# Performance work log

Hardware: AMD Instinct MI355X
Metric: run time of the kernel (lower is better)

## Reference

```python
import jax, jax.numpy as jnp
import numpy as np

B_, L_, D_MODEL = 2, 4096, 1024
D_STATE, D_CONV, D_INNER = 64, 4, 2048
EPS = 1.1920929e-07  # torch.finfo(float32).eps, nn.RMSNorm default


def setup_inputs() -> dict:
    key = jax.random.key(0)
    ks = jax.random.split(key, 8)
    s = 0.02
    x = jax.random.normal(ks[0], (B_, L_, D_MODEL), jnp.float32)
    W_in = jax.random.normal(ks[1], (D_MODEL, 2 * D_INNER), jnp.float32) * s
    conv_w = jax.random.normal(ks[2], (D_INNER, 1, D_CONV), jnp.float32) * s  # depthwise (O,I/g,K)
    conv_b = jnp.zeros((D_INNER,), jnp.float32)
    W_x = jax.random.normal(ks[3], (D_INNER, 2 * D_STATE + D_INNER), jnp.float32) * s
    W_dt = jax.random.normal(ks[4], (D_INNER, D_INNER), jnp.float32) * s
    b_dt = jnp.zeros((D_INNER,), jnp.float32)
    A_log = jnp.log(jnp.tile(jnp.arange(1, D_STATE + 1, dtype=jnp.float32)[None, :], (D_INNER, 1)))
    D_param = jnp.ones((D_INNER,), jnp.float32)
    W_out = jax.random.normal(ks[5], (D_INNER, D_MODEL), jnp.float32) * s
    norm_w = jnp.ones((D_INNER,), jnp.float32)
    return dict(x=x, W_in=W_in, conv_w=conv_w, conv_b=conv_b, W_x=W_x, W_dt=W_dt,
                b_dt=b_dt, A_log=A_log, D_param=D_param, W_out=W_out, norm_w=norm_w)


def selective_scan(x_conv, dt, A, B_ssm, C_ssm, D_param):
    # x_conv,dt: (B,L,d_inner); A:(d_inner,d_state); B_ssm,C_ssm:(B,L,d_state)
    dt = jax.nn.softplus(dt)

    def step(h, inp):
        dt_t, B_t, C_t, x_t = inp  # (B,di),(B,ds),(B,ds),(B,di)
        dA = jnp.exp(dt_t[:, :, None] * A[None, :, :])           # (B,di,ds)
        h = dA * h + (dt_t * x_t)[:, :, None] * B_t[:, None, :]  # (B,di,ds)
        y = jnp.einsum('bds,bs->bd', h, C_t)                     # (B,di)
        return h, y

    h0 = jnp.zeros((x_conv.shape[0], A.shape[0], A.shape[1]), x_conv.dtype)
    xs = (jnp.moveaxis(dt, 1, 0), jnp.moveaxis(B_ssm, 1, 0),
          jnp.moveaxis(C_ssm, 1, 0), jnp.moveaxis(x_conv, 1, 0))
    _, ys = jax.lax.scan(step, h0, xs)
    y = jnp.moveaxis(ys, 0, 1)  # (B,L,d_inner)
    return y + x_conv * D_param[None, None, :]


def reference(x, W_in, conv_w, conv_b, W_x, W_dt, b_dt, A_log, D_param, W_out, norm_w):
    xz = x @ W_in                                    # (B,L,2*d_inner)
    x_ssm, z = jnp.split(xz, 2, axis=-1)
    # causal depthwise conv1d: left-pad d_conv-1 == torch pad-both-then-slice[:L]
    xc = jnp.swapaxes(x_ssm, 1, 2)                   # (B,d_inner,L)
    xc = jax.lax.conv_general_dilated(
        xc, conv_w, window_strides=(1,), padding=[(D_CONV - 1, 0)],
        dimension_numbers=('NCH', 'OIH', 'NCH'), feature_group_count=D_INNER)
    xc = xc + conv_b[None, :, None]
    xc = jax.nn.silu(jnp.swapaxes(xc, 1, 2))         # (B,L,d_inner)
    dbc = xc @ W_x                                   # (B,L,2*d_state+d_inner)
    B_ssm = dbc[..., :D_STATE]
    C_ssm = dbc[..., D_STATE:2 * D_STATE]
    dt = dbc[..., 2 * D_STATE:] @ W_dt + b_dt
    A = -jnp.exp(A_log)
    y = selective_scan(xc, dt, A, B_ssm, C_ssm, D_param)
    # RMSNorm then gate
    y = y * jax.lax.rsqrt(jnp.mean(y * y, axis=-1, keepdims=True) + EPS) * norm_w
    y = y * jax.nn.silu(z)
    return y @ W_out
```

## Files before the change

### kernel.cpp

```cpp
#include <hip/hip_runtime.h>
#include <hip/hip_bf16.h>

#define L_SEQ   4096
#define DMODEL  1024
#define DINNER  2048
#define DSTATE  64
#define NB      2
#define DPB     128
#define NROWS   (NB * L_SEQ)

typedef unsigned short u16;
typedef __attribute__((ext_vector_type(8))) short bf16x8;
typedef __attribute__((ext_vector_type(4))) float f32x4;

__device__ __forceinline__ float silu_f(float x)  { return x / (1.f + __expf(-x)); }
__device__ __forceinline__ float softplus_f(float x) {
    return x > 15.f ? x : __logf(1.f + __expf(x));
}
__device__ __forceinline__ float bf2f(u16 u) { return __uint_as_float(((unsigned)u) << 16); }
__device__ __forceinline__ u16 f2bf(float f) {
    __hip_bfloat16 h = __float2bfloat16(f);
    return *reinterpret_cast<u16*>(&h);
}
__device__ __forceinline__ unsigned pack2(float a, float b) {
    return (unsigned)f2bf(a) | ((unsigned)f2bf(b) << 16);
}

__global__ __launch_bounds__(256) void f32_to_bf16_kernel(
    const float* __restrict__ in, u16* __restrict__ out)
{
    const int i = (blockIdx.x * 256 + threadIdx.x) * 4;
    float4 v = *reinterpret_cast<const float4*>(in + i);
    ushort4 o;
    o.x = f2bf(v.x); o.y = f2bf(v.y); o.z = f2bf(v.z); o.w = f2bf(v.w);
    *reinterpret_cast<ushort4*>(out + i) = o;
}

__global__ __launch_bounds__(256) void transpose_bf16_kernel(
    const float* __restrict__ W, u16* __restrict__ Wt, int K, int N)
{
    __shared__ float t[32][33];
    const int n0 = blockIdx.x * 32, k0 = blockIdx.y * 32;
    const int tx = threadIdx.x & 31, ty = threadIdx.x >> 5;
    #pragma unroll
    for (int i = 0; i < 32; i += 8)
        t[ty + i][tx] = W[(size_t)(k0 + ty + i) * N + n0 + tx];
    __syncthreads();
    #pragma unroll
    for (int i = 0; i < 32; i += 8)
        Wt[(size_t)(n0 + ty + i) * K + k0 + tx] = f2bf(t[tx][ty + i]);
}

__global__ __launch_bounds__(256) void bias_cat_kernel(
    const float* __restrict__ b_dt, float* __restrict__ bias)
{
    const int i = blockIdx.x * 256 + threadIdx.x;
    if (i < 128 + DINNER) bias[i] = (i < 128) ? 0.f : b_dt[i - 128];
}

template <typename TC>
__global__ __launch_bounds__(256) void mfma_gemm(
    const u16* __restrict__ A, int lda,
    const u16* __restrict__ Bt, int ldb,
    TC* __restrict__ C, int ldc,
    int K, const float* __restrict__ bias)
{
    __shared__ u16 As[128 * 32];
    __shared__ u16 Bs[128 * 32];
    const int tid  = threadIdx.x;
    const int lane = tid & 63;
    const int w    = tid >> 6;
    const int wm   = w >> 1, wn = w & 1;

    const int gx = gridDim.x;
    const int nwg = gx * gridDim.y;
    int wg = blockIdx.y * gx + blockIdx.x;
    if ((nwg & 7) == 0) wg = (wg & 7) * (nwg >> 3) + (wg >> 3);
    const int bm = (wg / gx) * 128, bn = (wg % gx) * 128;

    const int lr = lane & 15, lk = lane >> 4;
    const int srow  = lane >> 2;
    const int scolb = (lane & 3) * 16;
    const size_t ldaB = (size_t)lda * 2, ldbB = (size_t)ldb * 2;

    const char* Ab = (const char*)A + (size_t)bm * ldaB;
    const char* Bb = (const char*)Bt + (size_t)bn * ldbB;
    char* AsB = (char*)As;
    char* BsB = (char*)Bs;

    f32x4 acc[4][4] = {};

    for (int k0 = 0; k0 < K; k0 += 32) {
        const size_t kb = (size_t)k0 * 2;
        #pragma unroll
        for (int i = 0; i < 2; ++i) {
            const int row = i * 64 + w * 16 + srow;
            __builtin_amdgcn_global_load_lds(
                (const __attribute__((address_space(1))) void*)(Ab + (size_t)row * ldaB + kb + scolb),
                (__attribute__((address_space(3))) void*)(AsB + i * 4096 + w * 1024),
                16, 0, 0);
            __builtin_amdgcn_global_load_lds(
                (const __attribute__((address_space(1))) void*)(Bb + (size_t)row * ldbB + kb + scolb),
                (__attribute__((address_space(3))) void*)(BsB + i * 4096 + w * 1024),
                16, 0, 0);
        }
        __syncthreads();
        bf16x8 a[4], b[4];
        #pragma unroll
        for (int mi = 0; mi < 4; ++mi)
            a[mi] = *reinterpret_cast<const bf16x8*>(&As[(wm * 64 + mi * 16 + lr) * 32 + lk * 8]);
        #pragma unroll
        for (int ni = 0; ni < 4; ++ni)
            b[ni] = *reinterpret_cast<const bf16x8*>(&Bs[(wn * 64 + ni * 16 + lr) * 32 + lk * 8]);
        #pragma unroll
        for (int mi = 0; mi < 4; ++mi)
            #pragma unroll
            for (int ni = 0; ni < 4; ++ni)
                acc[mi][ni] = __builtin_amdgcn_mfma_f32_16x16x32_bf16(a[mi], b[ni], acc[mi][ni], 0, 0, 0);
        __syncthreads();
    }

    float bv[4];
    if (bias) {
        #pragma unroll
        for (int ni = 0; ni < 4; ++ni) bv[ni] = bias[bn + wn * 64 + ni * 16 + lr];
    }
    #pragma unroll
    for (int mi = 0; mi < 4; ++mi) {
        #pragma unroll
        for (int ni = 0; ni < 4; ++ni) {
            #pragma unroll
            for (int r = 0; r < 4; ++r) {
                const int row = bm + wm * 64 + mi * 16 + lk * 4 + r;
                const int col = bn + wn * 64 + ni * 16 + lr;
                float v = acc[mi][ni][r];
                if (bias) v += bv[ni];
                if constexpr (sizeof(TC) == 4) C[(size_t)row * ldc + col] = v;
                else                           C[(size_t)row * ldc + col] = f2bf(v);
            }
        }
    }
}

__global__ __launch_bounds__(256) void conv_silu_kernel(
    const u16* __restrict__ xz, const float* __restrict__ cw,
    const float* __restrict__ cb, u16* __restrict__ xc)
{
    const int idx8 = blockIdx.x * 256 + threadIdx.x;
    const int db  = (idx8 & 255) << 3;
    const int row = idx8 >> 8;
    const int l   = row & (L_SEQ - 1);

    float v[4][8];
    #pragma unroll
    for (int k = 0; k < 4; ++k) {
        const int ll = l - 3 + k;
        if (ll >= 0) {
            uint4 u = *reinterpret_cast<const uint4*>(xz + (size_t)(row - 3 + k) * 4096 + db);
            v[k][0]=bf2f((u16)(u.x&0xffff)); v[k][1]=bf2f((u16)(u.x>>16));
            v[k][2]=bf2f((u16)(u.y&0xffff)); v[k][3]=bf2f((u16)(u.y>>16));
            v[k][4]=bf2f((u16)(u.z&0xffff)); v[k][5]=bf2f((u16)(u.z>>16));
            v[k][6]=bf2f((u16)(u.w&0xffff)); v[k][7]=bf2f((u16)(u.w>>16));
        } else {
            #pragma unroll
            for (int j = 0; j < 8; ++j) v[k][j] = 0.f;
        }
    }
    float acc[8];
    {
        float4 c0 = *reinterpret_cast<const float4*>(cb + db);
        float4 c1 = *reinterpret_cast<const float4*>(cb + db + 4);
        acc[0]=c0.x; acc[1]=c0.y; acc[2]=c0.z; acc[3]=c0.w;
        acc[4]=c1.x; acc[5]=c1.y; acc[6]=c1.z; acc[7]=c1.w;
    }
    #pragma unroll
    for (int j = 0; j < 8; ++j) {
        const float4 wv = reinterpret_cast<const float4*>(cw)[db + j];
        acc[j] = fmaf(v[0][j], wv.x, acc[j]);
        acc[j] = fmaf(v[1][j], wv.y, acc[j]);
        acc[j] = fmaf(v[2][j], wv.z, acc[j]);
        acc[j] = fmaf(v[3][j], wv.w, acc[j]);
    }
    uint4 o;
    o.x = pack2(silu_f(acc[0]), silu_f(acc[1]));
    o.y = pack2(silu_f(acc[2]), silu_f(acc[3]));
    o.z = pack2(silu_f(acc[4]), silu_f(acc[5]));
    o.w = pack2(silu_f(acc[6]), silu_f(acc[7]));
    *reinterpret_cast<uint4*>(xc + (size_t)row * 2048 + db) = o;
}


__device__ __forceinline__ int a_pattern_check_half(
    const float* A_log, int d, int base, float& A0)
{
    A0 = -__expf(A_log[d * DSTATE]);
    int ok = 1;
    #pragma unroll
    for (int j = 0; j < 32; ++j) {
        const int s = base + j;
        const float As = -__expf(A_log[d * DSTATE + s]);
        ok &= (fabsf(As - A0 * (float)(s + 1)) <= 1e-3f * (float)(s + 1));
    }
    return ok;
}

#define UNPACK8(dstp, u)  do {                                             \
    float4 _a, _b;                                                         \
    _a.x=bf2f((u16)((u).x&0xffff)); _a.y=bf2f((u16)((u).x>>16));           \
    _a.z=bf2f((u16)((u).y&0xffff)); _a.w=bf2f((u16)((u).y>>16));           \
    _b.x=bf2f((u16)((u).z&0xffff)); _b.y=bf2f((u16)((u).z>>16));           \
    _b.z=bf2f((u16)((u).w&0xffff)); _b.w=bf2f((u16)((u).w>>16));           \
    *reinterpret_cast<float4*>(dstp) = _a;                                 \
    *reinterpret_cast<float4*>((dstp) + 4) = _b;                           \
} while (0)

#define UNPACK8_SP(dstp, u)  do {                                          \
    float4 _a, _b;                                                         \
    _a.x=softplus_f(bf2f((u16)((u).x&0xffff)));                            \
    _a.y=softplus_f(bf2f((u16)((u).x>>16)));                               \
    _a.z=softplus_f(bf2f((u16)((u).y&0xffff)));                            \
    _a.w=softplus_f(bf2f((u16)((u).y>>16)));                               \
    _b.x=softplus_f(bf2f((u16)((u).z&0xffff)));                            \
    _b.y=softplus_f(bf2f((u16)((u).z>>16)));                               \
    _b.z=softplus_f(bf2f((u16)((u).w&0xffff)));                            \
    _b.w=softplus_f(bf2f((u16)((u).w>>16)));                               \
    *reinterpret_cast<float4*>(dstp) = _a;                                 \
    *reinterpret_cast<float4*>((dstp) + 4) = _b;                           \
} while (0)

__global__ __launch_bounds__(256) void scan_phase1(
    const u16* __restrict__ xc,
    const u16* __restrict__ dbc,
    const float* __restrict__ A_log,
    float* __restrict__ hend, float* __restrict__ sumdt,
    int nchunk, int chunk)
{
    const int tid  = threadIdx.x;
    const int dl   = tid >> 1, half = tid & 1;
    const int base = half * 32;
    const int d0   = blockIdx.x * DPB;
    const int d    = d0 + dl;
    const int c = blockIdx.y, b = blockIdx.z;
    const int t0 = c * chunk;
    const size_t bL = (size_t)b * L_SEQ;

    __shared__ float dts_s[16][132];
    __shared__ float xcs_s[16][132];
    __shared__ float Bs_s[16][68];

    float A0;
    int fast = a_pattern_check_half(A_log, d, base, A0);
    fast = __syncthreads_and(fast);

    float h[32];
    #pragma unroll
    for (int j = 0; j < 32; ++j) h[j] = 0.f;
    float sd = 0.f;

    for (int ts = 0; ts < chunk; ts += 16) {
        __syncthreads();
        {
            const int rr = tid >> 4, cc = (tid & 15) * 8;
            const size_t row = bL + t0 + ts + rr;
            uint4 v = *reinterpret_cast<const uint4*>(dbc + row * 2176 + 128 + d0 + cc);
            UNPACK8_SP(&dts_s[rr][cc], v);
            uint4 u = *reinterpret_cast<const uint4*>(xc + row * 2048 + d0 + cc);
            UNPACK8(&xcs_s[rr][cc], u);
        }
        if (tid < 128) {
            const int rr = tid >> 3, cc = (tid & 7) * 8;
            const size_t row = bL + t0 + ts + rr;
            uint4 v = *reinterpret_cast<const uint4*>(dbc + row * 2176 + cc);
            UNPACK8(&Bs_s[rr][cc], v);
        }
        __syncthreads();
        if (fast) {
            for (int r = 0; r < 16; ++r) {
                const float dts = dts_s[r][dl];
                const float xv  = xcs_s[r][dl];
                const float dtx = dts * xv;
                sd += dts;
                const float q  = __expf(A0 * dts);
                const float q2 = q * q, q4 = q2 * q2;
                const float q8 = q4 * q4, q16 = q8 * q8, q32 = q16 * q16;
                const float qb = half ? q32 : 1.f;
                float p0 = qb * q, p1 = qb * q2, p2 = p1 * q, p3 = qb * q4;
                #pragma unroll
                for (int g = 0; g < 8; ++g) {
                    const float4 Bv = *reinterpret_cast<const float4*>(&Bs_s[r][base + g * 4]);
                    h[g*4+0] = fmaf(p0, h[g*4+0], dtx * Bv.x);
                    h[g*4+1] = fmaf(p1, h[g*4+1], dtx * Bv.y);
                    h[g*4+2] = fmaf(p2, h[g*4+2], dtx * Bv.z);
                    h[g*4+3] = fmaf(p3, h[g*4+3], dtx * Bv.w);
                    p0 *= q4; p1 *= q4; p2 *= q4; p3 *= q4;
                }
            }
        } else {
            for (int r = 0; r < 16; ++r) {
                const float dts = dts_s[r][dl];
                const float xv  = xcs_s[r][dl];
                const float dtx = dts * xv;
                sd += dts;
                #pragma unroll
                for (int j = 0; j < 32; ++j) {
                    const float a = __expf(-__expf(A_log[d * DSTATE + base + j]) * dts);
                    h[j] = fmaf(a, h[j], dtx * Bs_s[r][base + j]);
                }
            }
        }
    }
    const size_t cb64 = ((size_t)b * nchunk + c) * DSTATE;
    #pragma unroll
    for (int j = 0; j < 32; ++j) hend[(cb64 + base + j) * DINNER + d] = h[j];
    if (half == 0) sumdt[((size_t)b * nchunk + c) * DINNER + d] = sd;
}

__global__ __launch_bounds__(256) void scan_phase2(
    float* __restrict__ hbuf, const float* __restrict__ sumdt,
    const float* __restrict__ A_log, int nchunk)
{
    const int idx = blockIdx.x * 256 + threadIdx.x;
    const int d = idx & (DINNER - 1);
    const int s = (idx >> 11) & (DSTATE - 1);
    const int b = idx >> 17;

    const float A = -__expf(A_log[d * DSTATE + s]);
    float h = 0.f;
    for (int c = 0; c < nchunk; ++c) {
        const size_t off = (((size_t)b * nchunk + c) * DSTATE + s) * DINNER + d;
        const float he = hbuf[off];
        const float ap = __expf(A * sumdt[((size_t)b * nchunk + c) * DINNER + d]);
        hbuf[off] = h;
        h = fmaf(ap, h, he);
    }
}

__global__ __launch_bounds__(256) void scan_phase3(
    u16* __restrict__ xc,
    const u16* __restrict__ dbc,
    const float* __restrict__ A_log,
    const float* __restrict__ hinit,
    const float* __restrict__ D_param,
    int nchunk, int chunk)
{
    const int tid  = threadIdx.x;
    const int dl   = tid >> 1, half = tid & 1;
    const int base = half * 32;
    const int d0   = blockIdx.x * DPB;
    const int d    = d0 + dl;
    const int c = blockIdx.y, b = blockIdx.z;
    const int t0 = c * chunk;
    const size_t bL = (size_t)b * L_SEQ;

    __shared__ float dts_s[16][132];
    __shared__ float xcs_s[16][132];
    __shared__ float BCs[16][132];

    float A0;
    int fast = a_pattern_check_half(A_log, d, base, A0);
    fast = __syncthreads_and(fast);

    float h[32];
    {
        const size_t cb64 = ((size_t)b * nchunk + c) * DSTATE;
        #pragma unroll
        for (int j = 0; j < 32; ++j) h[j] = hinit[(cb64 + base + j) * DINNER + d];
    }
    const float Dp = D_param[d];

    for (int ts = 0; ts < chunk; ts += 16) {
        __syncthreads();
        {
            const int rr = tid >> 4, cc = (tid & 15) * 8;
            const size_t row = bL + t0 + ts + rr;
            uint4 v = *reinterpret_cast<const uint4*>(dbc + row * 2176 + 128 + d0 + cc);
            UNPACK8_SP(&dts_s[rr][cc], v);
            uint4 u = *reinterpret_cast<const uint4*>(xc + row * 2048 + d0 + cc);
            UNPACK8(&xcs_s[rr][cc], u);
            uint4 w = *reinterpret_cast<const uint4*>(dbc + row * 2176 + cc);
            UNPACK8(&BCs[rr][cc], w);
        }
        __syncthreads();
        if (fast) {
            for (int r = 0; r < 16; ++r) {
                const float dts = dts_s[r][dl];
                const float xv  = xcs_s[r][dl];
                const float dtx = dts * xv;
                const float q  = __expf(A0 * dts);
                const float q2 = q * q, q4 = q2 * q2;
                const float q8 = q4 * q4, q16 = q8 * q8, q32 = q16 * q16;
                const float qb = half ? q32 : 1.f;
                float p0 = qb * q, p1 = qb * q2, p2 = p1 * q, p3 = qb * q4;
                float y = 0.f;
                #pragma unroll
                for (int g = 0; g < 8; ++g) {
                    const float4 Bv = *reinterpret_cast<const float4*>(&BCs[r][base + g * 4]);
                    const float4 Cv = *reinterpret_cast<const float4*>(&BCs[r][64 + base + g * 4]);
                    h[g*4+0] = fmaf(p0, h[g*4+0], dtx * Bv.x);  y = fmaf(h[g*4+0], Cv.x, y);
                    h[g*4+1] = fmaf(p1, h[g*4+1], dtx * Bv.y);  y = fmaf(h[g*4+1], Cv.y, y);
                    h[g*4+2] = fmaf(p2, h[g*4+2], dtx * Bv.z);  y = fmaf(h[g*4+2], Cv.z, y);
                    h[g*4+3] = fmaf(p3, h[g*4+3], dtx * Bv.w);  y = fmaf(h[g*4+3], Cv.w, y);
                    p0 *= q4; p1 *= q4; p2 *= q4; p3 *= q4;
                }
                const float yt = y + __shfl_xor(y, 1, 64);
                if (half == 0) {
                    const size_t row = bL + t0 + ts + r;
                    xc[row * 2048 + d] = f2bf(fmaf(xv, Dp, yt));
                }
            }
        } else {
            for (int r = 0; r < 16; ++r) {
                const float dts = dts_s[r][dl];
                const float xv  = xcs_s[r][dl];
                const float dtx = dts * xv;
                float y = 0.f;
                #pragma unroll
                for (int j = 0; j < 32; ++j) {
                    const float a = __expf(-__expf(A_log[d * DSTATE + base + j]) * dts);
                    h[j] = fmaf(a, h[j], dtx * BCs[r][base + j]);
                    y = fmaf(h[j], BCs[r][64 + base + j], y);
                }
                const float yt = y + __shfl_xor(y, 1, 64);
                if (half == 0) {
                    const size_t row = bL + t0 + ts + r;
                    xc[row * 2048 + d] = f2bf(fmaf(xv, Dp, yt));
                }
            }
        }
    }
}

__global__ __launch_bounds__(256) void rms_gate_kernel(
    u16* __restrict__ y, const u16* __restrict__ xz,
    const float* __restrict__ norm_w)
{
    const int row = blockIdx.x;
    const int tid = threadIdx.x;
    const size_t ybase = (size_t)row * DINNER;
    const size_t zbase = (size_t)row * 4096 + DINNER;
    const int i8 = tid * 8;

    float yv[8];
    {
        uint4 u = *reinterpret_cast<const uint4*>(y + ybase + i8);
        yv[0]=bf2f((u16)(u.x&0xffff)); yv[1]=bf2f((u16)(u.x>>16));
        yv[2]=bf2f((u16)(u.y&0xffff)); yv[3]=bf2f((u16)(u.y>>16));
        yv[4]=bf2f((u16)(u.z&0xffff)); yv[5]=bf2f((u16)(u.z>>16));
        yv[6]=bf2f((u16)(u.w&0xffff)); yv[7]=bf2f((u16)(u.w>>16));
    }
    float ss = 0.f;
    #pragma unroll
    for (int j = 0; j < 8; ++j) ss = fmaf(yv[j], yv[j], ss);
    #pragma unroll
    for (int off = 32; off > 0; off >>= 1) ss += __shfl_down(ss, off, 64);
    __shared__ float sred[4];
    const int lane = tid & 63, wid = tid >> 6;
    if (lane == 0) sred[wid] = ss;
    __syncthreads();
    const float tot = sred[0] + sred[1] + sred[2] + sred[3];
    const float scale = rsqrtf(tot * (1.f / (float)DINNER) + 1.1920929e-07f);

    float zv[8];
    {
        uint4 u = *reinterpret_cast<const uint4*>(xz + zbase + i8);
        zv[0]=bf2f((u16)(u.x&0xffff)); zv[1]=bf2f((u16)(u.x>>16));
        zv[2]=bf2f((u16)(u.y&0xffff)); zv[3]=bf2f((u16)(u.y>>16));
        zv[4]=bf2f((u16)(u.z&0xffff)); zv[5]=bf2f((u16)(u.z>>16));
        zv[6]=bf2f((u16)(u.w&0xffff)); zv[7]=bf2f((u16)(u.w>>16));
    }
    float4 n0 = *reinterpret_cast<const float4*>(norm_w + i8);
    float4 n1 = *reinterpret_cast<const float4*>(norm_w + i8 + 4);
    const float nw[8] = {n0.x,n0.y,n0.z,n0.w,n1.x,n1.y,n1.z,n1.w};
    float o[8];
    #pragma unroll
    for (int j = 0; j < 8; ++j) o[j] = yv[j] * scale * nw[j] * silu_f(zv[j]);
    uint4 ov;
    ov.x = pack2(o[0], o[1]); ov.y = pack2(o[2], o[3]);
    ov.z = pack2(o[4], o[5]); ov.w = pack2(o[6], o[7]);
    *reinterpret_cast<uint4*>(y + ybase + i8) = ov;
}

extern "C" void kernel_launch(void* const* d_in, const int* in_sizes, int n_in,
                              void* d_out, int out_size, void* d_ws, size_t ws_size,
                              hipStream_t stream)
{
    const float* x       = (const float*)d_in[0];
    const float* W_in    = (const float*)d_in[1];
    const float* conv_w  = (const float*)d_in[2];
    const float* conv_b  = (const float*)d_in[3];
    const float* W_x     = (const float*)d_in[4];
    const float* W_dt    = (const float*)d_in[5];
    const float* b_dt    = (const float*)d_in[6];
    const float* A_log   = (const float*)d_in[7];
    const float* D_param = (const float*)d_in[8];
    const float* W_out   = (const float*)d_in[9];
    const float* norm_w  = (const float*)d_in[10];
    float* out = (float*)d_out;

    char* ws = (char*)d_ws;
    u16* xz  = (u16*)(ws);
    u16* xc  = (u16*)(ws + 67108864ull);
    u16* dbc = (u16*)(ws + 100663296ull);
    u16* xbf  = dbc;
    u16* Wxbf = xz;
    u16* Wt_out = (u16*)(ws + 136314880ull);
    float* bias2176 = (float*)(ws + 140509184ull);
    const size_t fixed_bytes = 140517888ull;
    const size_t per_chunk = 2ull * DSTATE * DINNER * 4 + 2ull * DINNER * 4;
    int nchunk = 64;
    while (nchunk > 1 && fixed_bytes + (size_t)nchunk * per_chunk > ws_size) nchunk >>= 1;
    const int chunk = L_SEQ / nchunk;
    float* hbuf = (float*)(ws + fixed_bytes);
    float* sdt  = (float*)(ws + fixed_bytes + (size_t)nchunk * 2ull * DSTATE * DINNER * 4);

    u16* Wt_in = (u16*)d_out;
    u16* Wt_x  = Wt_in + 4194304ull;
    u16* Wt_dt = Wt_x + 4456448ull;

    const int M = NROWS;

    f32_to_bf16_kernel<<<(M * DMODEL) / 1024, 256, 0, stream>>>(x, xbf);
    f32_to_bf16_kernel<<<(DINNER * 2176) / 1024, 256, 0, stream>>>(W_x, Wxbf);
    transpose_bf16_kernel<<<dim3(4096 / 32, 1024 / 32), 256, 0, stream>>>(W_in, Wt_in, 1024, 4096);
    transpose_bf16_kernel<<<dim3(4, 2048 / 32), 256, 0, stream>>>(W_x, Wt_x, 2048, 2176);
    transpose_bf16_kernel<<<dim3(2048 / 32, 2048 / 32), 256, 0, stream>>>(W_dt, Wt_dt, 2048, 2048);
    transpose_bf16_kernel<<<dim3(1024 / 32, 2048 / 32), 256, 0, stream>>>(W_out, Wt_out, 2048, 1024);
    bias_cat_kernel<<<9, 256, 0, stream>>>(b_dt, bias2176);
    mfma_gemm<u16><<<dim3(2048 / 128, 2048 / 128), 256, 0, stream>>>(
        Wt_dt, 2048, Wxbf + 128, 2176, Wt_x + 128ull * 2048, 2048, 2048, nullptr);

    mfma_gemm<u16><<<dim3(4096 / 128, M / 128), 256, 0, stream>>>(
        xbf, DMODEL, Wt_in, DMODEL, xz, 4096, DMODEL, nullptr);
    conv_silu_kernel<<<(M * DINNER) / (256 * 8), 256, 0, stream>>>(xz, conv_w, conv_b, xc);
    mfma_gemm<u16><<<dim3(2176 / 128, M / 128), 256, 0, stream>>>(
        xc, DINNER, Wt_x, DINNER, dbc, 2176, DINNER, bias2176);
    scan_phase1<<<dim3(DINNER / DPB, nchunk, NB), 256, 0, stream>>>(
        xc, dbc, A_log, hbuf, sdt, nchunk, chunk);
    scan_phase2<<<(NB * DINNER * DSTATE) / 256, 256, 0, stream>>>(hbuf, sdt, A_log, nchunk);
    scan_phase3<<<dim3(DINNER / DPB, nchunk, NB), 256, 0, stream>>>(
        xc, dbc, A_log, hbuf, D_param, nchunk, chunk);
    rms_gate_kernel<<<M, 256, 0, stream>>>(xc, xz, norm_w);
    mfma_gemm<float><<<dim3(1024 / 128, M / 128), 256, 0, stream>>>(
        xc, DINNER, Wt_out, DINNER, out, DMODEL, DINNER, nullptr);
}
```

Baseline: 675.5 us.

## Add 256x256 LDS-direct pipelined GEMM and fuse softplus into dt projection epilogue

Adds a new 512-thread GEMM kernel with 256x256 tiles, double-buffered LDS filled by direct global-to-LDS loads, swizzled layout, and interleaved load/MFMA phases with priority hints. It replaces the in-projection GEMM and the dt part of the x-projection GEMM. The dt columns are split into their own launch, and softplus is applied in that GEMM's epilogue. This removes per-element softplus from both scan phases and drops the bias concat kernel. Larger tiles aim to improve data reuse and overlap, at the cost of 128KB of LDS per block and an extra launch for the B/C columns.

```diff
diff --git a/kernel.cpp b/kernel.cpp
--- a/kernel.cpp
+++ b/kernel.cpp
@@ -49,13 +49,6 @@
     #pragma unroll
     for (int i = 0; i < 32; i += 8)
         Wt[(size_t)(n0 + ty + i) * K + k0 + tx] = f2bf(t[tx][ty + i]);
-}
-
-__global__ __launch_bounds__(256) void bias_cat_kernel(
-    const float* __restrict__ b_dt, float* __restrict__ bias)
-{
-    const int i = blockIdx.x * 256 + threadIdx.x;
-    if (i < 128 + DINNER) bias[i] = (i < 128) ? 0.f : b_dt[i - 128];
 }
 
 template <typename TC>
@@ -135,6 +128,178 @@
                 const int col = bn + wn * 64 + ni * 16 + lr;
                 float v = acc[mi][ni][r];
                 if (bias) v += bv[ni];
+                if constexpr (sizeof(TC) == 4) C[(size_t)row * ldc + col] = v;
+                else                           C[(size_t)row * ldc + col] = f2bf(v);
+            }
+        }
+    }
+}
+
+#define BAR()  asm volatile("s_barrier" ::: "memory")
+#define WV(n)  asm volatile("s_waitcnt vmcnt(" #n ")" ::: "memory")
+#define STG16(s, d) __builtin_amdgcn_global_load_lds( \
+    (const __attribute__((address_space(1))) void*)(s), \
+    (__attribute__((address_space(3))) void*)(d), 16, 0, 0)
+
+template <typename TC, int ACT>
+__global__ __launch_bounds__(512, 2) void gemm256(
+    const u16* __restrict__ A, int lda,
+    const u16* __restrict__ Bt, int ldb,
+    TC* __restrict__ C, int ldc,
+    int K, const float* __restrict__ bias)
+{
+    extern __shared__ char lds[];
+    const int tid = threadIdx.x;
+    const int l = tid & 63, w = tid >> 6;
+    const int wm = w >> 2, wn = w & 3;
+    const int lr = l & 15, lk = l >> 4;
+
+    const int gx = gridDim.x;
+    const int nwg = gx * gridDim.y;
+    int wg = blockIdx.y * gx + blockIdx.x;
+    wg = (wg & 7) * (nwg >> 3) + (wg >> 3);
+    const int bm = (wg / gx) * 256, bn = (wg % gx) * 256;
+
+    const size_t ldaB = (size_t)lda * 2, ldbB = (size_t)ldb * 2;
+    const int gsw = (((l & 7) ^ (l >> 3)) << 4);
+    const char* aSrc = (const char*)A + (size_t)(bm + w * 8 + (l >> 3)) * ldaB + gsw;
+    const char* bSrc = (const char*)Bt + (size_t)(bn + w * 8 + (l >> 3)) * ldbB + gsw;
+    const int csw0 = (lk * 16) ^ ((lr & 7) << 4);
+    const int wdst = w * 1024;
+
+    const int nk = K >> 6;
+    f32x4 acc[8][4] = {};
+
+    {
+        STG16(aSrc + (size_t)(0 * 64) * ldaB, lds + 0 * 8192 + wdst);
+        STG16(aSrc + (size_t)(2 * 64) * ldaB, lds + 2 * 8192 + wdst);
+        STG16(bSrc + (size_t)(0 * 64) * ldbB, lds + 32768 + 0 * 8192 + wdst);
+        STG16(bSrc + (size_t)(1 * 64) * ldbB, lds + 32768 + 1 * 8192 + wdst);
+        STG16(bSrc + (size_t)(2 * 64) * ldbB, lds + 32768 + 2 * 8192 + wdst);
+        STG16(bSrc + (size_t)(3 * 64) * ldbB, lds + 32768 + 3 * 8192 + wdst);
+        STG16(aSrc + (size_t)(1 * 64) * ldaB, lds + 1 * 8192 + wdst);
+        STG16(aSrc + (size_t)(3 * 64) * ldaB, lds + 3 * 8192 + wdst);
+        WV(2);
+        BAR();
+    }
+
+    for (int t = 0; t < nk; ++t) {
+        const int p = t & 1;
+        const char* Ar = lds + (p << 16);
+        const char* Br = Ar + 32768;
+        const int tn = (t + 1 < nk) ? t + 1 : t;
+        char* dq = lds + (((t + 1) & 1) << 16);
+        const size_t Tb = (size_t)tn << 7;
+        const char* aS = aSrc + Tb;
+        const char* bS = bSrc + Tb;
+
+        bf16x8 a[4][2], bf[2][2];
+
+        #pragma unroll
+        for (int mi = 0; mi < 4; ++mi) {
+            const int ro = (wm * 128 + mi * 16 + lr) * 128;
+            a[mi][0] = *reinterpret_cast<const bf16x8*>(Ar + ro + csw0);
+            a[mi][1] = *reinterpret_cast<const bf16x8*>(Ar + ro + (csw0 ^ 64));
+        }
+        #pragma unroll
+        for (int ni = 0; ni < 2; ++ni) {
+            const int ro = (wn * 64 + ni * 16 + lr) * 128;
+            bf[ni][0] = *reinterpret_cast<const bf16x8*>(Br + ro + csw0);
+            bf[ni][1] = *reinterpret_cast<const bf16x8*>(Br + ro + (csw0 ^ 64));
+        }
+        STG16(aS + (size_t)(0 * 64) * ldaB, dq + 0 * 8192 + wdst);
+        STG16(aS + (size_t)(2 * 64) * ldaB, dq + 2 * 8192 + wdst);
+        BAR();
+        __builtin_amdgcn_s_setprio(1);
+        #pragma unroll
+        for (int mi = 0; mi < 4; ++mi)
+            #pragma unroll
+            for (int ni = 0; ni < 2; ++ni) {
+                acc[mi][ni] = __builtin_amdgcn_mfma_f32_16x16x32_bf16(a[mi][0], bf[ni][0], acc[mi][ni], 0, 0, 0);
+                acc[mi][ni] = __builtin_amdgcn_mfma_f32_16x16x32_bf16(a[mi][1], bf[ni][1], acc[mi][ni], 0, 0, 0);
+            }
+        __builtin_amdgcn_s_setprio(0);
+        BAR();
+
+        #pragma unroll
+        for (int ni = 0; ni < 2; ++ni) {
+            const int ro = (wn * 64 + (2 + ni) * 16 + lr) * 128;
+            bf[ni][0] = *reinterpret_cast<const bf16x8*>(Br + ro + csw0);
+            bf[ni][1] = *reinterpret_cast<const bf16x8*>(Br + ro + (csw0 ^ 64));
+        }
+        STG16(bS + (size_t)(0 * 64) * ldbB, dq + 32768 + 0 * 8192 + wdst);
+        STG16(bS + (size_t)(1 * 64) * ldbB, dq + 32768 + 1 * 8192 + wdst);
+        BAR();
+        __builtin_amdgcn_s_setprio(1);
+        #pragma unroll
+        for (int mi = 0; mi < 4; ++mi)
+            #pragma unroll
+            for (int ni = 0; ni < 2; ++ni) {
+                acc[mi][2 + ni] = __builtin_amdgcn_mfma_f32_16x16x32_bf16(a[mi][0], bf[ni][0], acc[mi][2 + ni], 0, 0, 0);
+                acc[mi][2 + ni] = __builtin_amdgcn_mfma_f32_16x16x32_bf16(a[mi][1], bf[ni][1], acc[mi][2 + ni], 0, 0, 0);
+            }
+        __builtin_amdgcn_s_setprio(0);
+        WV(4);
+        BAR();
+
+        #pragma unroll
+        for (int mi = 0; mi < 4; ++mi) {
+            const int ro = (wm * 128 + (4 + mi) * 16 + lr) * 128;
+            a[mi][0] = *reinterpret_cast<const bf16x8*>(Ar + ro + csw0);
+            a[mi][1] = *reinterpret_cast<const bf16x8*>(Ar + ro + (csw0 ^ 64));
+        }
+        STG16(bS + (size_t)(2 * 64) * ldbB, dq + 32768 + 2 * 8192 + wdst);
+        STG16(bS + (size_t)(3 * 64) * ldbB, dq + 32768 + 3 * 8192 + wdst);
+        BAR();
+        __builtin_amdgcn_s_setprio(1);
+        #pragma unroll
+        for (int mi = 0; mi < 4; ++mi)
+            #pragma unroll
+            for (int ni = 0; ni < 2; ++ni) {
+                acc[4 + mi][2 + ni] = __builtin_amdgcn_mfma_f32_16x16x32_bf16(a[mi][0], bf[ni][0], acc[4 + mi][2 + ni], 0, 0, 0);
+                acc[4 + mi][2 + ni] = __builtin_amdgcn_mfma_f32_16x16x32_bf16(a[mi][1], bf[ni][1], acc[4 + mi][2 + ni], 0, 0, 0);
+            }
+        __builtin_amdgcn_s_setprio(0);
+        BAR();
+
+        #pragma unroll
+        for (int ni = 0; ni < 2; ++ni) {
+            const int ro = (wn * 64 + ni * 16 + lr) * 128;
+            bf[ni][0] = *reinterpret_cast<const bf16x8*>(Br + ro + csw0);
+            bf[ni][1] = *reinterpret_cast<const bf16x8*>(Br + ro + (csw0 ^ 64));
+        }
+        STG16(aS + (size_t)(1 * 64) * ldaB, dq + 1 * 8192 + wdst);
+        STG16(aS + (size_t)(3 * 64) * ldaB, dq + 3 * 8192 + wdst);
+        BAR();
+        __builtin_amdgcn_s_setprio(1);
+        #pragma unroll
+        for (int mi = 0; mi < 4; ++mi)
+            #pragma unroll
+            for (int ni = 0; ni < 2; ++ni) {
+                acc[4 + mi][ni] = __builtin_amdgcn_mfma_f32_16x16x32_bf16(a[mi][0], bf[ni][0], acc[4 + mi][ni], 0, 0, 0);
+                acc[4 + mi][ni] = __builtin_amdgcn_mfma_f32_16x16x32_bf16(a[mi][1], bf[ni][1], acc[4 + mi][ni], 0, 0, 0);
+            }
+        __builtin_amdgcn_s_setprio(0);
+        WV(2);
+        BAR();
+    }
+
+    float bv[4];
+    if (bias) {
+        #pragma unroll
+        for (int ni = 0; ni < 4; ++ni) bv[ni] = bias[bn + wn * 64 + ni * 16 + lr];
+    }
+    #pragma unroll
+    for (int mi = 0; mi < 8; ++mi) {
+        #pragma unroll
+        for (int ni = 0; ni < 4; ++ni) {
+            #pragma unroll
+            for (int r = 0; r < 4; ++r) {
+                const int row = bm + wm * 128 + mi * 16 + lk * 4 + r;
+                const int col = bn + wn * 64 + ni * 16 + lr;
+                float v = acc[mi][ni][r];
+                if (bias) v += bv[ni];
+                if constexpr (ACT == 1) v = softplus_f(v);
                 if constexpr (sizeof(TC) == 4) C[(size_t)row * ldc + col] = v;
                 else                           C[(size_t)row * ldc + col] = f2bf(v);
             }
@@ -214,20 +379,6 @@
     *reinterpret_cast<float4*>((dstp) + 4) = _b;                           \
 } while (0)
 
-#define UNPACK8_SP(dstp, u)  do {                                          \
-    float4 _a, _b;                                                         \
-    _a.x=softplus_f(bf2f((u16)((u).x&0xffff)));                            \
-    _a.y=softplus_f(bf2f((u16)((u).x>>16)));                               \
-    _a.z=softplus_f(bf2f((u16)((u).y&0xffff)));                            \
-    _a.w=softplus_f(bf2f((u16)((u).y>>16)));                               \
-    _b.x=softplus_f(bf2f((u16)((u).z&0xffff)));                            \
-    _b.y=softplus_f(bf2f((u16)((u).z>>16)));                               \
-    _b.z=softplus_f(bf2f((u16)((u).w&0xffff)));                            \
-    _b.w=softplus_f(bf2f((u16)((u).w>>16)));                               \
-    *reinterpret_cast<float4*>(dstp) = _a;                                 \
-    *reinterpret_cast<float4*>((dstp) + 4) = _b;                           \
-} while (0)
-
 __global__ __launch_bounds__(256) void scan_phase1(
     const u16* __restrict__ xc,
     const u16* __restrict__ dbc,
@@ -263,7 +414,7 @@
             const int rr = tid >> 4, cc = (tid & 15) * 8;
             const size_t row = bL + t0 + ts + rr;
             uint4 v = *reinterpret_cast<const uint4*>(dbc + row * 2176 + 128 + d0 + cc);
-            UNPACK8_SP(&dts_s[rr][cc], v);
+            UNPACK8(&dts_s[rr][cc], v);
             uint4 u = *reinterpret_cast<const uint4*>(xc + row * 2048 + d0 + cc);
             UNPACK8(&xcs_s[rr][cc], u);
         }
@@ -374,7 +525,7 @@
             const int rr = tid >> 4, cc = (tid & 15) * 8;
             const size_t row = bL + t0 + ts + rr;
             uint4 v = *reinterpret_cast<const uint4*>(dbc + row * 2176 + 128 + d0 + cc);
-            UNPACK8_SP(&dts_s[rr][cc], v);
+            UNPACK8(&dts_s[rr][cc], v);
             uint4 u = *reinterpret_cast<const uint4*>(xc + row * 2048 + d0 + cc);
             UNPACK8(&xcs_s[rr][cc], u);
             uint4 w = *reinterpret_cast<const uint4*>(dbc + row * 2176 + cc);
@@ -497,6 +648,11 @@
     const float* norm_w  = (const float*)d_in[10];
     float* out = (float*)d_out;
 
+    hipFuncSetAttribute(reinterpret_cast<const void*>(&gemm256<u16, 0>),
+                        hipFuncAttributeMaxDynamicSharedMemorySize, 131072);
+    hipFuncSetAttribute(reinterpret_cast<const void*>(&gemm256<u16, 1>),
+                        hipFuncAttributeMaxDynamicSharedMemorySize, 131072);
+
     char* ws = (char*)d_ws;
     u16* xz  = (u16*)(ws);
     u16* xc  = (u16*)(ws + 67108864ull);
@@ -504,8 +660,7 @@
     u16* xbf  = dbc;
     u16* Wxbf = xz;
     u16* Wt_out = (u16*)(ws + 136314880ull);
-    float* bias2176 = (float*)(ws + 140509184ull);
-    const size_t fixed_bytes = 140517888ull;
+    const size_t fixed_bytes = 140509184ull;
     const size_t per_chunk = 2ull * DSTATE * DINNER * 4 + 2ull * DINNER * 4;
     int nchunk = 64;
     while (nchunk > 1 && fixed_bytes + (size_t)nchunk * per_chunk > ws_size) nchunk >>= 1;
@@ -525,15 +680,16 @@
     transpose_bf16_kernel<<<dim3(4, 2048 / 32), 256, 0, stream>>>(W_x, Wt_x, 2048, 2176);
     transpose_bf16_kernel<<<dim3(2048 / 32, 2048 / 32), 256, 0, stream>>>(W_dt, Wt_dt, 2048, 2048);
     transpose_bf16_kernel<<<dim3(1024 / 32, 2048 / 32), 256, 0, stream>>>(W_out, Wt_out, 2048, 1024);
-    bias_cat_kernel<<<9, 256, 0, stream>>>(b_dt, bias2176);
     mfma_gemm<u16><<<dim3(2048 / 128, 2048 / 128), 256, 0, stream>>>(
         Wt_dt, 2048, Wxbf + 128, 2176, Wt_x + 128ull * 2048, 2048, 2048, nullptr);
 
-    mfma_gemm<u16><<<dim3(4096 / 128, M / 128), 256, 0, stream>>>(
+    gemm256<u16, 0><<<dim3(4096 / 256, M / 256), 512, 131072, stream>>>(
         xbf, DMODEL, Wt_in, DMODEL, xz, 4096, DMODEL, nullptr);
     conv_silu_kernel<<<(M * DINNER) / (256 * 8), 256, 0, stream>>>(xz, conv_w, conv_b, xc);
-    mfma_gemm<u16><<<dim3(2176 / 128, M / 128), 256, 0, stream>>>(
-        xc, DINNER, Wt_x, DINNER, dbc, 2176, DINNER, bias2176);
+    mfma_gemm<u16><<<dim3(1, M / 128), 256, 0, stream>>>(
+        xc, DINNER, Wt_x, DINNER, dbc, 2176, DINNER, nullptr);
+    gemm256<u16, 1><<<dim3(2048 / 256, M / 256), 512, 131072, stream>>>(
+        xc, DINNER, Wt_x + 128ull * 2048, DINNER, dbc + 128, 2176, DINNER, b_dt);
     scan_phase1<<<dim3(DINNER / DPB, nchunk, NB), 256, 0, stream>>>(
         xc, dbc, A_log, hbuf, sdt, nchunk, chunk);
     scan_phase2<<<(NB * DINNER * DSTATE) / 256, 256, 0, stream>>>(hbuf, sdt, A_log, nchunk);
```

Result: faster. 653.3 us (-3.3%).
